# Kernel optimization log

Measured on AMD Instinct MI355X. Metric: run time of the kernel, lower is better.

## Reference

```python
import jax, jax.numpy as jnp
import numpy as np

B, L, D, K, P, V = 64, 512, 768, 2, 128, 2048
HID = D + K * P  # 1024, concat of token-path and position-path
N_TYPES, FEAT, TGT, PAD = 8, 5, 6, 1
EPS = 1e-12


def setup_inputs() -> dict:
    key = jax.random.key(0)
    ks = jax.random.split(key, 24)
    s = 0.02

    def tab(k, n, d, zero_row):
        t = jax.random.normal(k, (n, d), jnp.float32) * s
        return t.at[zero_row].set(0.0) if zero_row is not None else t

    inp = {
        "input_ids": jax.random.randint(ks[0], (B, L), 0, V, jnp.int32),
        "token_type_ids": jax.random.randint(ks[1], (B, L), 0, N_TYPES, jnp.int32),
        "pos_embed_ids": jax.random.randint(ks[2], (B, L, K), 0, L, jnp.int32),
        "lp_embeds": jax.random.normal(ks[3], (B, L, P), jnp.float32),
        "prop_atom_in_ring": jax.random.randint(ks[4], (B, L), 0, 3, jnp.int32),
        "prop_atom_charge": jax.random.randint(ks[5], (B, L), 0, 4, jnp.int32),
        "prop_atom_hybridization": jax.random.randint(ks[6], (B, L), 0, 9, jnp.int32),
        "prop_atom_chirality": jax.random.randint(ks[7], (B, L), 0, 5, jnp.int32),
        "prop_bond_aromatic": jax.random.randint(ks[8], (B, L), 0, 3, jnp.int32),
        "prop_bond_conjugated": jax.random.randint(ks[9], (B, L), 0, 3, jnp.int32),
        "prop_bond_stereo": jax.random.randint(ks[10], (B, L), 0, 7, jnp.int32),
        "mol_features": jax.random.uniform(ks[11], (B, L), jnp.float32),
        "target_values": jax.random.normal(ks[12], (B, L), jnp.float32),
        # learned parameters (padding rows zeroed to match padding_idx semantics)
        "emb_table": tab(ks[13], V, D, PAD),
        "type_table": tab(ks[14], N_TYPES, D, None),
        "ring_tab": tab(ks[15], 3, D, 0),
        "charge_tab": tab(ks[16], 4, D, 0),
        "hyb_tab": tab(ks[17], 9, D, 0),
        "chir_tab": tab(ks[18], 5, D, 0),
        "arom_tab": tab(ks[19], 3, D, 0),
        "conj_tab": tab(ks[20], 3, D, 0),
        "stereo_tab": tab(ks[21], 7, D, 0),
        "ln_gamma": jnp.ones((HID,), jnp.float32),
        "ln_beta": jnp.zeros((HID,), jnp.float32),
    }
    return inp


def reference(input_ids, token_type_ids, pos_embed_ids, lp_embeds,
              prop_atom_in_ring, prop_atom_charge, prop_atom_hybridization,
              prop_atom_chirality, prop_bond_aromatic, prop_bond_conjugated,
              prop_bond_stereo, mol_features, target_values,
              emb_table, type_table, ring_tab, charge_tab, hyb_tab, chir_tab,
              arom_tab, conj_tab, stereo_tab, ln_gamma, ln_beta):
    # position path (no-grad in original; eval mode: no random sign flip)
    lp = jnp.nan_to_num(lp_embeds, nan=0.0)
    # per-batch gather: lp[b, pos_embed_ids[b,l,k], :] -> [B,L,K,P]
    pos = jax.vmap(lambda ids, e: e[ids])(pos_embed_ids, lp)
    pos = pos.reshape(B, L, K * P)

    tok = emb_table[input_ids]                      # [B,L,D]
    feat_mask = (token_type_ids == FEAT)[..., None]
    tok = tok + jnp.where(feat_mask, tok * mol_features[..., None], 0.0)
    tgt_mask = (token_type_ids == TGT)[..., None]
    tok = tok + jnp.where(tgt_mask, tok * target_values[..., None], 0.0)

    # property embeddings; row 0 is zero so dense lookup == sparse select
    prop = (ring_tab[prop_atom_in_ring] + charge_tab[prop_atom_charge]
            + hyb_tab[prop_atom_hybridization] + chir_tab[prop_atom_chirality]
            + arom_tab[prop_bond_aromatic] + conj_tab[prop_bond_conjugated]
            + stereo_tab[prop_bond_stereo])

    emb = jnp.concatenate([tok + type_table[token_type_ids] + prop, pos], axis=-1)

    mu = jnp.mean(emb, axis=-1, keepdims=True)
    var = jnp.mean(jnp.square(emb - mu), axis=-1, keepdims=True)
    out = (emb - mu) * jax.lax.rsqrt(var + EPS) * ln_gamma + ln_beta
    return out  # dropout prob 0 / eval mode
```

## Files before the change

### kernel.cpp

```cpp
#include <hip/hip_runtime.h>
#include <math.h>

#define NB   64
#define NL   512
#define ND   768
#define NP   128
#define NHID 1024
#define NTOK (NB * NL)

__device__ __forceinline__ float4 f4add(float4 a, float4 b) {
    return make_float4(a.x + b.x, a.y + b.y, a.z + b.z, a.w + b.w);
}

__device__ __forceinline__ float nanfix(float x) { return (x == x) ? x : 0.0f; }

__device__ __forceinline__ float wave_sum(float x) {
    #pragma unroll
    for (int off = 32; off > 0; off >>= 1) x += __shfl_xor(x, off, 64);
    return x;
}

__global__ __launch_bounds__(256)
void molt_embed_ln(
    const int*   __restrict__ input_ids,
    const int*   __restrict__ token_type_ids,
    const int*   __restrict__ pos_embed_ids,
    const float* __restrict__ lp_embeds,
    const int*   __restrict__ p_ring,
    const int*   __restrict__ p_charge,
    const int*   __restrict__ p_hyb,
    const int*   __restrict__ p_chir,
    const int*   __restrict__ p_arom,
    const int*   __restrict__ p_conj,
    const int*   __restrict__ p_stereo,
    const float* __restrict__ mol_features,
    const float* __restrict__ target_values,
    const float* __restrict__ emb_table,
    const float* __restrict__ type_table,
    const float* __restrict__ ring_tab,
    const float* __restrict__ charge_tab,
    const float* __restrict__ hyb_tab,
    const float* __restrict__ chir_tab,
    const float* __restrict__ arom_tab,
    const float* __restrict__ conj_tab,
    const float* __restrict__ stereo_tab,
    const float* __restrict__ ln_gamma,
    const float* __restrict__ ln_beta,
    float*       __restrict__ out)
{
    const int lane = threadIdx.x & 63;
    int t = (blockIdx.x << 2) + (threadIdx.x >> 6);
    t = __builtin_amdgcn_readfirstlane(t);
    const int b = t >> 9;

    const int id   = input_ids[t];
    const int tt   = token_type_ids[t];
    const int ir   = p_ring[t];
    const int ic   = p_charge[t];
    const int ihy  = p_hyb[t];
    const int ichr = p_chir[t];
    const int ia   = p_arom[t];
    const int icj  = p_conj[t];
    const int ist  = p_stereo[t];

    float scale = 1.0f;
    if (tt == 5)      scale = 1.0f + mol_features[t];
    else if (tt == 6) scale = 1.0f + target_values[t];

    const int h0 = lane * 12;
    const float4* e  = (const float4*)(emb_table  + (size_t)id   * ND + h0);
    const float4* ty = (const float4*)(type_table + (size_t)tt   * ND + h0);
    const float4* r  = (const float4*)(ring_tab   + (size_t)ir   * ND + h0);
    const float4* c  = (const float4*)(charge_tab + (size_t)ic   * ND + h0);
    const float4* hy = (const float4*)(hyb_tab    + (size_t)ihy  * ND + h0);
    const float4* ch = (const float4*)(chir_tab   + (size_t)ichr * ND + h0);
    const float4* ar = (const float4*)(arom_tab   + (size_t)ia   * ND + h0);
    const float4* cj = (const float4*)(conj_tab   + (size_t)icj  * ND + h0);
    const float4* st = (const float4*)(stereo_tab + (size_t)ist  * ND + h0);

    float4 v[4];
    #pragma unroll
    for (int j = 0; j < 3; ++j) {
        float4 a = e[j];
        float4 s = f4add(f4add(f4add(ty[j], r[j]), f4add(c[j], hy[j])),
                         f4add(f4add(ch[j], ar[j]), f4add(cj[j], st[j])));
        float4 q;
        q.x = fmaf(a.x, scale, s.x);
        q.y = fmaf(a.y, scale, s.y);
        q.z = fmaf(a.z, scale, s.z);
        q.w = fmaf(a.w, scale, s.w);
        v[j] = q;
    }

    {
        const int local = lane << 2;
        const int kk    = local >> 7;
        const int pp    = local & 127;
        const int pid   = pos_embed_ids[(t << 1) + kk];
        float4 a = *(const float4*)(lp_embeds + ((size_t)(b * NL + pid)) * NP + pp);
        a.x = nanfix(a.x); a.y = nanfix(a.y); a.z = nanfix(a.z); a.w = nanfix(a.w);
        v[3] = a;
    }

    float s = 0.0f;
    #pragma unroll
    for (int j = 0; j < 4; ++j) s += v[j].x + v[j].y + v[j].z + v[j].w;
    s = wave_sum(s);
    const float mean = s * (1.0f / (float)NHID);

    float q2 = 0.0f;
    #pragma unroll
    for (int j = 0; j < 4; ++j) {
        float dx = v[j].x - mean, dy = v[j].y - mean,
              dz = v[j].z - mean, dw = v[j].w - mean;
        q2 += dx * dx + dy * dy + dz * dz + dw * dw;
    }
    q2 = wave_sum(q2);
    const float var = q2 * (1.0f / (float)NHID);
    const float inv = 1.0f / sqrtf(var + 1e-12f);

    float* orow = out + (size_t)t * NHID;
    const float4* g0 = (const float4*)(ln_gamma + h0);
    const float4* b0 = (const float4*)(ln_beta  + h0);
    float4* o0 = (float4*)(orow + h0);
    #pragma unroll
    for (int j = 0; j < 3; ++j) {
        float4 g = g0[j], be = b0[j], q;
        q.x = fmaf((v[j].x - mean) * inv, g.x, be.x);
        q.y = fmaf((v[j].y - mean) * inv, g.y, be.y);
        q.z = fmaf((v[j].z - mean) * inv, g.z, be.z);
        q.w = fmaf((v[j].w - mean) * inv, g.w, be.w);
        o0[j] = q;
    }
    {
        const int hp = ND + (lane << 2);
        float4 g = *(const float4*)(ln_gamma + hp);
        float4 be = *(const float4*)(ln_beta + hp);
        float4 q;
        q.x = fmaf((v[3].x - mean) * inv, g.x, be.x);
        q.y = fmaf((v[3].y - mean) * inv, g.y, be.y);
        q.z = fmaf((v[3].z - mean) * inv, g.z, be.z);
        q.w = fmaf((v[3].w - mean) * inv, g.w, be.w);
        *(float4*)(orow + hp) = q;
    }
}

extern "C" void kernel_launch(void* const* d_in, const int* in_sizes, int n_in,
                              void* d_out, int out_size, void* d_ws, size_t ws_size,
                              hipStream_t stream) {
    (void)in_sizes; (void)n_in; (void)out_size; (void)d_ws; (void)ws_size;
    molt_embed_ln<<<NTOK / 4, 256, 0, stream>>>(
        (const int*)d_in[0],  (const int*)d_in[1],  (const int*)d_in[2],
        (const float*)d_in[3],
        (const int*)d_in[4],  (const int*)d_in[5],  (const int*)d_in[6],
        (const int*)d_in[7],  (const int*)d_in[8],  (const int*)d_in[9],
        (const int*)d_in[10],
        (const float*)d_in[11], (const float*)d_in[12],
        (const float*)d_in[13], (const float*)d_in[14], (const float*)d_in[15],
        (const float*)d_in[16], (const float*)d_in[17], (const float*)d_in[18],
        (const float*)d_in[19], (const float*)d_in[20], (const float*)d_in[21],
        (const float*)d_in[22], (const float*)d_in[23],
        (float*)d_out);
}
```

Baseline: 255.7 us.

## Process two tokens per wave with single-pass LN stats and nontemporal stores

Each wave now handles two consecutive tokens, and the grid is halved. This adds memory-level parallelism and amortises gamma/beta loads and shuffle reductions across both tokens. LayerNorm statistics are computed in one pass (sum and sum of squares, clamped at zero), which removes the second reduction round. Output writes use nontemporal stores so the large output does not pollute the cache, at the cost of more registers and slightly weaker numerical stability for the variance.

```diff
diff --git a/kernel.cpp b/kernel.cpp
--- a/kernel.cpp
+++ b/kernel.cpp
@@ -8,17 +8,7 @@
 #define NHID 1024
 #define NTOK (NB * NL)
 
-__device__ __forceinline__ float4 f4add(float4 a, float4 b) {
-    return make_float4(a.x + b.x, a.y + b.y, a.z + b.z, a.w + b.w);
-}
-
-__device__ __forceinline__ float nanfix(float x) { return (x == x) ? x : 0.0f; }
-
-__device__ __forceinline__ float wave_sum(float x) {
-    #pragma unroll
-    for (int off = 32; off > 0; off >>= 1) x += __shfl_xor(x, off, 64);
-    return x;
-}
+typedef float f4 __attribute__((ext_vector_type(4)));
 
 __global__ __launch_bounds__(256)
 void molt_embed_ln(
@@ -49,99 +39,99 @@
     float*       __restrict__ out)
 {
     const int lane = threadIdx.x & 63;
-    int t = (blockIdx.x << 2) + (threadIdx.x >> 6);
-    t = __builtin_amdgcn_readfirstlane(t);
-    const int b = t >> 9;
+    int t0 = (blockIdx.x << 3) + ((threadIdx.x >> 6) << 1);
+    t0 = __builtin_amdgcn_readfirstlane(t0);
+    const int t1 = t0 + 1;
+    const int b  = t0 >> 9;
+    const int h0 = lane * 12;
 
-    const int id   = input_ids[t];
-    const int tt   = token_type_ids[t];
-    const int ir   = p_ring[t];
-    const int ic   = p_charge[t];
-    const int ihy  = p_hyb[t];
-    const int ichr = p_chir[t];
-    const int ia   = p_arom[t];
-    const int icj  = p_conj[t];
-    const int ist  = p_stereo[t];
+    f4 v0[4], v1[4];
 
-    float scale = 1.0f;
-    if (tt == 5)      scale = 1.0f + mol_features[t];
-    else if (tt == 6) scale = 1.0f + target_values[t];
+    auto tok = [&](int t, f4* v) {
+        const int id   = input_ids[t];
+        const int tt   = token_type_ids[t];
+        const int ir   = p_ring[t];
+        const int ic   = p_charge[t];
+        const int ihy  = p_hyb[t];
+        const int ichr = p_chir[t];
+        const int ia   = p_arom[t];
+        const int icj  = p_conj[t];
+        const int ist  = p_stereo[t];
 
-    const int h0 = lane * 12;
-    const float4* e  = (const float4*)(emb_table  + (size_t)id   * ND + h0);
-    const float4* ty = (const float4*)(type_table + (size_t)tt   * ND + h0);
-    const float4* r  = (const float4*)(ring_tab   + (size_t)ir   * ND + h0);
-    const float4* c  = (const float4*)(charge_tab + (size_t)ic   * ND + h0);
-    const float4* hy = (const float4*)(hyb_tab    + (size_t)ihy  * ND + h0);
-    const float4* ch = (const float4*)(chir_tab   + (size_t)ichr * ND + h0);
-    const float4* ar = (const float4*)(arom_tab   + (size_t)ia   * ND + h0);
-    const float4* cj = (const float4*)(conj_tab   + (size_t)icj  * ND + h0);
-    const float4* st = (const float4*)(stereo_tab + (size_t)ist  * ND + h0);
+        float scale = 1.0f;
+        if (tt == 5)      scale += mol_features[t];
+        else if (tt == 6) scale += target_values[t];
 
-    float4 v[4];
+        const f4* e  = (const f4*)(emb_table  + (size_t)id   * ND + h0);
+        const f4* ty = (const f4*)(type_table + (size_t)tt   * ND + h0);
+        const f4* r  = (const f4*)(ring_tab   + (size_t)ir   * ND + h0);
+        const f4* c  = (const f4*)(charge_tab + (size_t)ic   * ND + h0);
+        const f4* hy = (const f4*)(hyb_tab    + (size_t)ihy  * ND + h0);
+        const f4* ch = (const f4*)(chir_tab   + (size_t)ichr * ND + h0);
+        const f4* ar = (const f4*)(arom_tab   + (size_t)ia   * ND + h0);
+        const f4* cj = (const f4*)(conj_tab   + (size_t)icj  * ND + h0);
+        const f4* st = (const f4*)(stereo_tab + (size_t)ist  * ND + h0);
+
+        #pragma unroll
+        for (int j = 0; j < 3; ++j) {
+            f4 s = ty[j] + r[j] + c[j] + hy[j] + ch[j] + ar[j] + cj[j] + st[j];
+            v[j] = e[j] * scale + s;
+        }
+
+        const int kk  = lane >> 5;
+        const int pp  = (lane & 31) << 2;
+        const int pid = pos_embed_ids[(t << 1) + kk];
+        f4 a = *(const f4*)(lp_embeds + ((size_t)(b * NL + pid)) * NP + pp);
+        #pragma unroll
+        for (int k = 0; k < 4; ++k) a[k] = (a[k] == a[k]) ? a[k] : 0.0f;
+        v[3] = a;
+    };
+    tok(t0, v0);
+    tok(t1, v1);
+
+    float s0 = 0.f, p0 = 0.f, s1 = 0.f, p1 = 0.f;
+    #pragma unroll
+    for (int j = 0; j < 4; ++j) {
+        #pragma unroll
+        for (int k = 0; k < 4; ++k) {
+            float a = v0[j][k], c = v1[j][k];
+            s0 += a; p0 += a * a;
+            s1 += c; p1 += c * c;
+        }
+    }
+    #pragma unroll
+    for (int off = 32; off; off >>= 1) {
+        s0 += __shfl_xor(s0, off, 64);
+        s1 += __shfl_xor(s1, off, 64);
+        p0 += __shfl_xor(p0, off, 64);
+        p1 += __shfl_xor(p1, off, 64);
+    }
+    const float mean0 = s0 * (1.0f / (float)NHID);
+    const float mean1 = s1 * (1.0f / (float)NHID);
+    const float var0  = fmaxf(p0 * (1.0f / (float)NHID) - mean0 * mean0, 0.0f);
+    const float var1  = fmaxf(p1 * (1.0f / (float)NHID) - mean1 * mean1, 0.0f);
+    const float inv0  = 1.0f / sqrtf(var0 + 1e-12f);
+    const float inv1  = 1.0f / sqrtf(var1 + 1e-12f);
+
+    float* o0 = out + (size_t)t0 * NHID;
+    float* o1 = out + (size_t)t1 * NHID;
     #pragma unroll
     for (int j = 0; j < 3; ++j) {
-        float4 a = e[j];
-        float4 s = f4add(f4add(f4add(ty[j], r[j]), f4add(c[j], hy[j])),
-                         f4add(f4add(ch[j], ar[j]), f4add(cj[j], st[j])));
-        float4 q;
-        q.x = fmaf(a.x, scale, s.x);
-        q.y = fmaf(a.y, scale, s.y);
-        q.z = fmaf(a.z, scale, s.z);
-        q.w = fmaf(a.w, scale, s.w);
-        v[j] = q;
-    }
-
-    {
-        const int local = lane << 2;
-        const int kk    = local >> 7;
-        const int pp    = local & 127;
-        const int pid   = pos_embed_ids[(t << 1) + kk];
-        float4 a = *(const float4*)(lp_embeds + ((size_t)(b * NL + pid)) * NP + pp);
-        a.x = nanfix(a.x); a.y = nanfix(a.y); a.z = nanfix(a.z); a.w = nanfix(a.w);
-        v[3] = a;
-    }
-
-    float s = 0.0f;
-    #pragma unroll
-    for (int j = 0; j < 4; ++j) s += v[j].x + v[j].y + v[j].z + v[j].w;
-    s = wave_sum(s);
-    const float mean = s * (1.0f / (float)NHID);
-
-    float q2 = 0.0f;
-    #pragma unroll
-    for (int j = 0; j < 4; ++j) {
-        float dx = v[j].x - mean, dy = v[j].y - mean,
-              dz = v[j].z - mean, dw = v[j].w - mean;
-        q2 += dx * dx + dy * dy + dz * dz + dw * dw;
-    }
-    q2 = wave_sum(q2);
-    const float var = q2 * (1.0f / (float)NHID);
-    const float inv = 1.0f / sqrtf(var + 1e-12f);
-
-    float* orow = out + (size_t)t * NHID;
-    const float4* g0 = (const float4*)(ln_gamma + h0);
-    const float4* b0 = (const float4*)(ln_beta  + h0);
-    float4* o0 = (float4*)(orow + h0);
-    #pragma unroll
-    for (int j = 0; j < 3; ++j) {
-        float4 g = g0[j], be = b0[j], q;
-        q.x = fmaf((v[j].x - mean) * inv, g.x, be.x);
-        q.y = fmaf((v[j].y - mean) * inv, g.y, be.y);
-        q.z = fmaf((v[j].z - mean) * inv, g.z, be.z);
-        q.w = fmaf((v[j].w - mean) * inv, g.w, be.w);
-        o0[j] = q;
+        f4 g  = *(const f4*)(ln_gamma + h0 + 4 * j);
+        f4 be = *(const f4*)(ln_beta  + h0 + 4 * j);
+        f4 q0 = (v0[j] - mean0) * inv0 * g + be;
+        f4 q1 = (v1[j] - mean1) * inv1 * g + be;
+        __builtin_nontemporal_store(q0, (f4*)(o0 + h0 + 4 * j));
+        __builtin_nontemporal_store(q1, (f4*)(o1 + h0 + 4 * j));
     }
     {
         const int hp = ND + (lane << 2);
-        float4 g = *(const float4*)(ln_gamma + hp);
-        float4 be = *(const float4*)(ln_beta + hp);
-        float4 q;
-        q.x = fmaf((v[3].x - mean) * inv, g.x, be.x);
-        q.y = fmaf((v[3].y - mean) * inv, g.y, be.y);
-        q.z = fmaf((v[3].z - mean) * inv, g.z, be.z);
-        q.w = fmaf((v[3].w - mean) * inv, g.w, be.w);
-        *(float4*)(orow + hp) = q;
+        f4 g  = *(const f4*)(ln_gamma + hp);
+        f4 be = *(const f4*)(ln_beta  + hp);
+        f4 q0 = (v0[3] - mean0) * inv0 * g + be;
+        f4 q1 = (v1[3] - mean1) * inv1 * g + be;
+        __builtin_nontemporal_store(q0, (f4*)(o0 + hp));
+        __builtin_nontemporal_store(q1, (f4*)(o1 + hp));
     }
 }
 
@@ -149,7 +139,7 @@
                               void* d_out, int out_size, void* d_ws, size_t ws_size,
                               hipStream_t stream) {
     (void)in_sizes; (void)n_in; (void)out_size; (void)d_ws; (void)ws_size;
-    molt_embed_ln<<<NTOK / 4, 256, 0, stream>>>(
+    molt_embed_ln<<<NTOK / 8, 256, 0, stream>>>(
         (const int*)d_in[0],  (const int*)d_in[1],  (const int*)d_in[2],
         (const float*)d_in[3],
         (const int*)d_in[4],  (const int*)d_in[5],  (const int*)d_in[6],
```

Measured after the change: 281.9 us. 1.1x slower.
